# Kernel optimization log

Measured on AMD Instinct MI355X. Metric: run time of the kernel, lower is better.

The kernel has to match this reference:

```python
import jax, jax.numpy as jnp
import numpy as np

# Module hyperparameters (from init_kwargs)
THRESHOLD_BASE = 1.0
TAU_MEM, TAU_SYN, TAU_ADAPT = 0.02, 0.005, 0.1
ADAPT_STRENGTH, HOMEO_RATE, DT = 0.1, 0.01, 0.001


def setup_inputs() -> dict:
    key = jax.random.key(0)
    B, F, T = 32, 8192, 128
    input_current = jax.random.normal(key, (B, F, T), dtype=jnp.float32)
    threshold_scale = jnp.ones((1,), dtype=jnp.float32)   # nn.Parameter(torch.ones(1))
    adaptation_bias = jnp.zeros((1,), dtype=jnp.float32)  # nn.Parameter(torch.zeros(1))
    return {"input_current": input_current,
            "threshold_scale": threshold_scale,
            "adaptation_bias": adaptation_bias}


def reference(input_current, threshold_scale, adaptation_bias):
    """Adaptive-threshold LIF neuron recurrence (AdaptiveThresholdLIFNeuron.forward).

    input_current: [B, F, T]
    Returns (spikes [B,F,T], membrane_trace [T], threshold_trace [T],
             final_firing_rate (scalar EMA), adaptation_state (scalar mean)).
    """
    B, F, T = input_current.shape
    dt = jnp.float32(DT)
    alpha = jnp.exp(-dt / TAU_MEM)   # membrane decay
    beta = jnp.exp(-dt / TAU_SYN)    # synaptic decay
    gamma = jnp.exp(-dt / TAU_ADAPT) # adaptation decay

    I_t = jnp.moveaxis(input_current, -1, 0)  # [T, B, F] for scan over time

    def step(carry, inp):
        membrane, synaptic, adaptation, ema = carry
        synaptic = beta * synaptic + inp
        membrane = alpha * membrane + synaptic
        # homeostatic component uses the running firing-rate EMA (scalar buffer)
        homeo = ADAPT_STRENGTH * jnp.maximum(ema - HOMEO_RATE, 0.0)
        adaptation = gamma * adaptation + (1.0 - gamma) * jax.lax.stop_gradient(membrane)
        threshold = (THRESHOLD_BASE * threshold_scale + homeo
                     + adaptation_bias + 0.1 * adaptation)  # [B, F]
        spike = (membrane >= threshold).astype(membrane.dtype)
        ema = 0.99 * ema + 0.01 * spike.mean()
        membrane = membrane - threshold * spike  # soft reset
        return (membrane, synaptic, adaptation, ema), (spike, membrane.mean(), threshold.mean())

    z = jnp.zeros((B, F), dtype=input_current.dtype)
    init = (z, z, z, jnp.zeros((), dtype=input_current.dtype))
    (membrane, synaptic, adaptation, ema), (spikes_t, mem_trace, thr_trace) = jax.lax.scan(step, init, I_t)

    spikes = jnp.moveaxis(spikes_t, 0, -1)  # [B, F, T]
    return spikes, mem_trace, thr_trace, ema, adaptation.mean()
```

## Files before the change

kernel.cpp:

```cpp
#include <hip/hip_runtime.h>
#include <math.h>

#pragma clang fp contract(off)

typedef unsigned int u32;
typedef unsigned long long u64;

#define N_NEUR 262144
#define TT     128
#define OB     ((size_t)N_NEUR * TT)
#define PB     128
#define PT     512
#define NW     8
#define WGUARD (1 << 16)
#define MGUARD (1 << 17)

__device__ __forceinline__ float wredf(float v) {
#pragma unroll
  for (int o = 32; o; o >>= 1) v += __shfl_xor(v, o);
  return v;
}
__device__ __forceinline__ int wredi(int v) {
#pragma unroll
  for (int o = 32; o; o >>= 1) v += __shfl_xor(v, o);
  return v;
}

__launch_bounds__(PT)
__global__ void snn_persist(const float* __restrict__ in, const float* __restrict__ tsp,
                            const float* __restrict__ abp, float* __restrict__ out,
                            u32* __restrict__ bits2, u32* __restrict__ g_cnt,
                            u64* __restrict__ g_sc, float* __restrict__ wm,
                            float* __restrict__ wt, float* __restrict__ wa)
{
#pragma clang fp contract(off)
  const int tid  = threadIdx.x;
  const int bid  = blockIdx.x;
  const int lane = tid & 63;
  const int wv   = tid >> 6;

  if (bid == PB) {
    if (wv != 0) return;
    const float tsv = tsp[0], abv = abp[0];
    float ema = 0.0f;
    for (int t = 0; t < TT; ++t) {
      const u32* slots = g_cnt + (size_t)t * PB;
      u32 v0, v1; int gd = 0;
      while (1) {
        v0 = __hip_atomic_load(&slots[lane],      __ATOMIC_RELAXED, __HIP_MEMORY_SCOPE_AGENT);
        v1 = __hip_atomic_load(&slots[lane + 64], __ATOMIC_RELAXED, __HIP_MEMORY_SCOPE_AGENT);
        if (__all(v0 != 0u && v1 != 0u)) break;
        if (++gd > MGUARD) break;
      }
      int ss = (int)(v0 ? v0 - 1u : 0u) + (int)(v1 ? v1 - 1u : 0u);
      ss = wredi(ss);
      const float mean = (float)ss * 3.814697265625e-06f;
      ema = __builtin_fmaf(0.99f, ema, 0.01f * mean);
      if (t < TT - 1) {
        const float scn = (tsv + 0.1f * fmaxf(ema - 0.01f, 0.0f)) + abv;
        const u64 pkt = ((u64)__float_as_uint(scn) << 32) | 1ull;
        if (lane < 16)
          __hip_atomic_store(&g_sc[(size_t)(t + 1) * 16 + lane], pkt,
                             __ATOMIC_RELAXED, __HIP_MEMORY_SCOPE_AGENT);
      }
    }
    if (lane == 0) out[OB + 256] = ema;
    return;
  }

  const int gtid = bid * PT + tid;

  const float alp = __uint_as_float(0x3F7383C5u);
  const float bet = __uint_as_float(0x3F519856u);
  const float gma = __uint_as_float(0x3F7D73E8u);
  const float omg = 1.0f - gma;
  const float tsv = tsp[0];
  const float abv = abp[0];

  const int n0 = gtid * 4;
  const float4* q0 = (const float4*)(in + (size_t)(n0 + 0) * TT);
  const float4* q1 = (const float4*)(in + (size_t)(n0 + 1) * TT);
  const float4* q2 = (const float4*)(in + (size_t)(n0 + 2) * TT);
  const float4* q3 = (const float4*)(in + (size_t)(n0 + 3) * TT);

  float4 c0 = q0[0], c1 = q1[0], c2 = q2[0], c3 = q3[0];
  float4 f0 = q0[1], f1 = q1[1], f2 = q2[1], f3 = q3[1];

  float S0,S1,S2,S3, Mp0,Mp1,Mp2,Mp3, A0,A1,A2,A3;
  S0 = __builtin_fmaf(bet, 0.0f, c0.x); Mp0 = __builtin_fmaf(alp, 0.0f, S0);
  A0 = __builtin_fmaf(gma, 0.0f, omg * Mp0);
  S1 = __builtin_fmaf(bet, 0.0f, c1.x); Mp1 = __builtin_fmaf(alp, 0.0f, S1);
  A1 = __builtin_fmaf(gma, 0.0f, omg * Mp1);
  S2 = __builtin_fmaf(bet, 0.0f, c2.x); Mp2 = __builtin_fmaf(alp, 0.0f, S2);
  A2 = __builtin_fmaf(gma, 0.0f, omg * Mp2);
  S3 = __builtin_fmaf(bet, 0.0f, c3.x); Mp3 = __builtin_fmaf(alp, 0.0f, S3);
  A3 = __builtin_fmaf(gma, 0.0f, omg * Mp3);

  float sc;
  { const float homeo = 0.1f * fmaxf(0.0f - 0.01f, 0.0f);
    sc = (tsv + homeo) + abv; }

  __shared__ int   shc[NW];
  __shared__ float shm[NW];
  __shared__ u32   s_sc;

  float M0, M1, M2, M3;

#define STEP(T_, IN0, IN1, IN2, IN3) {                                         \
    if ((T_) > 0) {                                                            \
      if (tid == 0) {                                                          \
        u64 v_; int gd_ = 0;                                                   \
        while (1) {                                                            \
          v_ = __hip_atomic_load(&g_sc[(size_t)(T_) * 16 + (bid & 15)],        \
                                 __ATOMIC_RELAXED, __HIP_MEMORY_SCOPE_AGENT);  \
          if ((u32)v_ != 0u) break;                                            \
          if (++gd_ > WGUARD) break;                                           \
          __builtin_amdgcn_s_sleep(1);                                         \
        }                                                                      \
        s_sc = (u32)(v_ >> 32);                                                \
      }                                                                        \
      __syncthreads();                                                         \
      sc = __uint_as_float(s_sc);                                              \
    }                                                                          \
    const float th0 = __builtin_fmaf(0.1f, A0, sc);                            \
    const float th1 = __builtin_fmaf(0.1f, A1, sc);                            \
    const float th2 = __builtin_fmaf(0.1f, A2, sc);                            \
    const float th3 = __builtin_fmaf(0.1f, A3, sc);                            \
    const bool sp0 = (Mp0 >= th0);  M0 = sp0 ? Mp0 - th0 : Mp0;                \
    const bool sp1 = (Mp1 >= th1);  M1 = sp1 ? Mp1 - th1 : Mp1;                \
    const bool sp2 = (Mp2 >= th2);  M2 = sp2 ? Mp2 - th2 : Mp2;                \
    const bool sp3 = (Mp3 >= th3);  M3 = sp3 ? Mp3 - th3 : Mp3;                \
    int cnt = (int)sp0 + (int)sp1 + (int)sp2 + (int)sp3;                       \
    cnt = wredi(cnt);                                                          \
    if (lane == 0) shc[wv] = cnt;                                              \
    __syncthreads();                                                           \
    if (tid == 0) {                                                            \
      const int bc = ((((((shc[0] + shc[1]) + shc[2]) + shc[3]) + shc[4])      \
                       + shc[5]) + shc[6]) + shc[7];                           \
      __hip_atomic_store(&g_cnt[(size_t)(T_) * PB + bid], (u32)bc + 1u,        \
                         __ATOMIC_RELAXED, __HIP_MEMORY_SCOPE_AGENT);          \
    }                                                                          \
                                       \
    u32 nib = (u32)sp0 | ((u32)sp1 << 1) | ((u32)sp2 << 2) | ((u32)sp3 << 3);  \
    u32 word = nib << (4 * (tid & 7));                                         \
    word |= (u32)__shfl_xor((int)word, 1);                                     \
    word |= (u32)__shfl_xor((int)word, 2);                                     \
    word |= (u32)__shfl_xor((int)word, 4);                                     \
    if ((tid & 7) == 0) bits2[(size_t)(gtid >> 3) * TT + (T_)] = word;         \
    float msum = ((M0 + M1) + M2) + M3;                                        \
    float tsum = ((th0 + th1) + th2) + th3;                                    \
    msum = wredf(msum); tsum = wredf(tsum);                                    \
    if (lane == 0) {                                                           \
      wm[((size_t)(T_) * PB + bid) * NW + wv] = msum;                          \
      wt[((size_t)(T_) * PB + bid) * NW + wv] = tsum;                          \
    }                                                                          \
    if ((T_) < TT - 1) {             \
      S0 = __builtin_fmaf(bet, S0, (IN0));                                     \
      Mp0 = __builtin_fmaf(alp, M0, S0);                                       \
      A0 = __builtin_fmaf(gma, A0, omg * Mp0);                                 \
      S1 = __builtin_fmaf(bet, S1, (IN1));                                     \
      Mp1 = __builtin_fmaf(alp, M1, S1);                                       \
      A1 = __builtin_fmaf(gma, A1, omg * Mp1);                                 \
      S2 = __builtin_fmaf(bet, S2, (IN2));                                     \
      Mp2 = __builtin_fmaf(alp, M2, S2);                                       \
      A2 = __builtin_fmaf(gma, A2, omg * Mp2);                                 \
      S3 = __builtin_fmaf(bet, S3, (IN3));                                     \
      Mp3 = __builtin_fmaf(alp, M3, S3);                                       \
      A3 = __builtin_fmaf(gma, A3, omg * Mp3);                                 \
    }                                                                          \
  }

#pragma unroll 1
  for (int q = 0; q < 32; ++q) {
    float4 p0 = {0,0,0,0}, p1 = {0,0,0,0}, p2 = {0,0,0,0}, p3 = {0,0,0,0};
    if (q < 30) { p0 = q0[q + 2]; p1 = q1[q + 2]; p2 = q2[q + 2]; p3 = q3[q + 2]; }
    const int tb = 4 * q;
    STEP(tb + 0, c0.y, c1.y, c2.y, c3.y)
    STEP(tb + 1, c0.z, c1.z, c2.z, c3.z)
    STEP(tb + 2, c0.w, c1.w, c2.w, c3.w)
    STEP(tb + 3, f0.x, f1.x, f2.x, f3.x)
    c0 = f0; c1 = f1; c2 = f2; c3 = f3;
    f0 = p0; f1 = p1; f2 = p2; f3 = p3;
  }
#undef STEP

  float asum = ((A0 + A1) + A2) + A3;
  asum = wredf(asum);
  if (lane == 0) shm[wv] = asum;
  __syncthreads();
  if (tid == 0) {
    float bs = 0.f;
    for (int w = 0; w < NW; ++w) bs += shm[w];
    wa[bid] = bs;
  }
}

__launch_bounds__(256)
__global__ void snn_finish(const float* __restrict__ wm, const float* __restrict__ wt,
                           const float* __restrict__ wa, float* __restrict__ out)
{
#pragma clang fp contract(off)
  const int tid = threadIdx.x;
  const float inv = 3.814697265625e-06f;
  if (tid < 128) {
    float s = 0.f;
    for (int j = 0; j < PB * NW; ++j) s += wm[(size_t)tid * PB * NW + j];
    out[OB + tid] = s * inv;
  } else {
    const int t = tid - 128;
    float s = 0.f;
    for (int j = 0; j < PB * NW; ++j) s += wt[(size_t)t * PB * NW + j];
    out[OB + 128 + t] = s * inv;
  }
  if (tid == 0) {
    float s = 0.f;
    for (int b = 0; b < PB; ++b) s += wa[b];
    out[OB + 257] = s * inv;
  }
}

__global__ void snn_expand(const u32* __restrict__ bits2, float* __restrict__ outF)
{
  const int gtid = blockIdx.x * blockDim.x + threadIdx.x;
  const int wave = gtid >> 6, lane = gtid & 63;
  const int nwaves = (gridDim.x * blockDim.x) >> 6;
  const int nloc = lane >> 5;
  const int tq   = lane & 31;
  for (int pair = wave; pair < N_NEUR / 2; pair += nwaves) {
    const int n = 2 * pair + nloc;
    const uint4 w = *(const uint4*)(bits2 + (size_t)(n >> 5) * TT + 4 * tq);
    const int b = n & 31;
    float4 f;
    f.x = (float)((w.x >> b) & 1u);
    f.y = (float)((w.y >> b) & 1u);
    f.z = (float)((w.z >> b) & 1u);
    f.w = (float)((w.w >> b) & 1u);
    ((float4*)outF)[(size_t)n * (TT / 4) + tq] = f;
  }
}

extern "C" void kernel_launch(void* const* d_in, const int* in_sizes, int n_in,
                              void* d_out, int out_size, void* d_ws, size_t ws_size,
                              hipStream_t stream)
{
  const float* in  = (const float*)d_in[0];
  const float* tsp = (const float*)d_in[1];
  const float* abp = (const float*)d_in[2];
  float* out = (float*)d_out;
  unsigned char* ws = (unsigned char*)d_ws;

  if (ws_size < 5326000u) return;

  u32*   bits2 = (u32*)(ws);
  float* wm    = (float*)(ws + 4194304);
  float* wt    = (float*)(ws + 4718592);
  u32*   g_cnt = (u32*)(ws + 5242880);
  u64*   g_sc  = (u64*)(ws + 5308416);
  float* wa    = (float*)(ws + 5324800);

  hipMemsetAsync(g_cnt, 0, 81920, stream);

  snn_persist<<<dim3(PB + 1), dim3(PT), 0, stream>>>(in, tsp, abp, out,
                                                     bits2, g_cnt, g_sc, wm, wt, wa);
  snn_finish<<<dim3(1), dim3(256), 0, stream>>>(wm, wt, wa, out);
  snn_expand<<<dim3(2048), dim3(256), 0, stream>>>(bits2, out);
}
```

Measured before the change: 383.2 us.

## Replace master-block EMA broadcast with replicated all-to-all spike count exchange

Drops the dedicated master block that gathered per-block spike counts and broadcast the new threshold scale. Each block now writes its count into 16 replicated slot arrays, and one wavefront per block polls all 128 counts from its replica and computes the EMA locally. This removes one serial hop (gather, then broadcast) from the per-timestep critical path. In exchange it adds more global polling traffic, a larger memset, and an extra __syncthreads per step.

```diff
diff --git a/kernel.cpp b/kernel.cpp
--- a/kernel.cpp
+++ b/kernel.cpp
@@ -4,7 +4,6 @@
 #pragma clang fp contract(off)
 
 typedef unsigned int u32;
-typedef unsigned long long u64;
 
 #define N_NEUR 262144
 #define TT     128
@@ -12,8 +11,8 @@
 #define PB     128
 #define PT     512
 #define NW     8
-#define WGUARD (1 << 16)
-#define MGUARD (1 << 17)
+#define NREP   16
+#define WGUARD (1 << 17)
 
 __device__ __forceinline__ float wredf(float v) {
 #pragma unroll
@@ -29,46 +28,17 @@
 __launch_bounds__(PT)
 __global__ void snn_persist(const float* __restrict__ in, const float* __restrict__ tsp,
                             const float* __restrict__ abp, float* __restrict__ out,
-                            u32* __restrict__ bits2, u32* __restrict__ g_cnt,
-                            u64* __restrict__ g_sc, float* __restrict__ wm,
-                            float* __restrict__ wt, float* __restrict__ wa)
+                            u32* __restrict__ bits2, u32* __restrict__ g_rep,
+                            float* __restrict__ wm, float* __restrict__ wt,
+                            float* __restrict__ wa)
 {
 #pragma clang fp contract(off)
   const int tid  = threadIdx.x;
   const int bid  = blockIdx.x;
+  const int gtid = bid * PT + tid;
   const int lane = tid & 63;
   const int wv   = tid >> 6;
-
-  if (bid == PB) {
-    if (wv != 0) return;
-    const float tsv = tsp[0], abv = abp[0];
-    float ema = 0.0f;
-    for (int t = 0; t < TT; ++t) {
-      const u32* slots = g_cnt + (size_t)t * PB;
-      u32 v0, v1; int gd = 0;
-      while (1) {
-        v0 = __hip_atomic_load(&slots[lane],      __ATOMIC_RELAXED, __HIP_MEMORY_SCOPE_AGENT);
-        v1 = __hip_atomic_load(&slots[lane + 64], __ATOMIC_RELAXED, __HIP_MEMORY_SCOPE_AGENT);
-        if (__all(v0 != 0u && v1 != 0u)) break;
-        if (++gd > MGUARD) break;
-      }
-      int ss = (int)(v0 ? v0 - 1u : 0u) + (int)(v1 ? v1 - 1u : 0u);
-      ss = wredi(ss);
-      const float mean = (float)ss * 3.814697265625e-06f;
-      ema = __builtin_fmaf(0.99f, ema, 0.01f * mean);
-      if (t < TT - 1) {
-        const float scn = (tsv + 0.1f * fmaxf(ema - 0.01f, 0.0f)) + abv;
-        const u64 pkt = ((u64)__float_as_uint(scn) << 32) | 1ull;
-        if (lane < 16)
-          __hip_atomic_store(&g_sc[(size_t)(t + 1) * 16 + lane], pkt,
-                             __ATOMIC_RELAXED, __HIP_MEMORY_SCOPE_AGENT);
-      }
-    }
-    if (lane == 0) out[OB + 256] = ema;
-    return;
-  }
-
-  const int gtid = bid * PT + tid;
+  const int rep  = bid & (NREP - 1);
 
   const float alp = __uint_as_float(0x3F7383C5u);
   const float bet = __uint_as_float(0x3F519856u);
@@ -96,32 +66,16 @@
   S3 = __builtin_fmaf(bet, 0.0f, c3.x); Mp3 = __builtin_fmaf(alp, 0.0f, S3);
   A3 = __builtin_fmaf(gma, 0.0f, omg * Mp3);
 
-  float sc;
-  { const float homeo = 0.1f * fmaxf(0.0f - 0.01f, 0.0f);
-    sc = (tsv + homeo) + abv; }
+  float ema = 0.0f;
+  float sc  = (tsv + 0.1f * fmaxf(0.0f - 0.01f, 0.0f)) + abv;
 
   __shared__ int   shc[NW];
   __shared__ float shm[NW];
-  __shared__ u32   s_sc;
+  __shared__ u32   s_tot;
 
   float M0, M1, M2, M3;
 
 #define STEP(T_, IN0, IN1, IN2, IN3) {                                         \
-    if ((T_) > 0) {                                                            \
-      if (tid == 0) {                                                          \
-        u64 v_; int gd_ = 0;                                                   \
-        while (1) {                                                            \
-          v_ = __hip_atomic_load(&g_sc[(size_t)(T_) * 16 + (bid & 15)],        \
-                                 __ATOMIC_RELAXED, __HIP_MEMORY_SCOPE_AGENT);  \
-          if ((u32)v_ != 0u) break;                                            \
-          if (++gd_ > WGUARD) break;                                           \
-          __builtin_amdgcn_s_sleep(1);                                         \
-        }                                                                      \
-        s_sc = (u32)(v_ >> 32);                                                \
-      }                                                                        \
-      __syncthreads();                                                         \
-      sc = __uint_as_float(s_sc);                                              \
-    }                                                                          \
     const float th0 = __builtin_fmaf(0.1f, A0, sc);                            \
     const float th1 = __builtin_fmaf(0.1f, A1, sc);                            \
     const float th2 = __builtin_fmaf(0.1f, A2, sc);                            \
@@ -134,13 +88,14 @@
     cnt = wredi(cnt);                                                          \
     if (lane == 0) shc[wv] = cnt;                                              \
     __syncthreads();                                                           \
-    if (tid == 0) {                                                            \
+    if (tid < NREP) {   \
       const int bc = ((((((shc[0] + shc[1]) + shc[2]) + shc[3]) + shc[4])      \
                        + shc[5]) + shc[6]) + shc[7];                           \
-      __hip_atomic_store(&g_cnt[(size_t)(T_) * PB + bid], (u32)bc + 1u,        \
+      __hip_atomic_store(&g_rep[((size_t)(T_) * NREP + tid) * PB + bid],       \
+                         (u32)bc + 1u,                                         \
                          __ATOMIC_RELAXED, __HIP_MEMORY_SCOPE_AGENT);          \
     }                                                                          \
-                                       \
+                        \
     u32 nib = (u32)sp0 | ((u32)sp1 << 1) | ((u32)sp2 << 2) | ((u32)sp3 << 3);  \
     u32 word = nib << (4 * (tid & 7));                                         \
     word |= (u32)__shfl_xor((int)word, 1);                                     \
@@ -168,6 +123,26 @@
       Mp3 = __builtin_fmaf(alp, M3, S3);                                       \
       A3 = __builtin_fmaf(gma, A3, omg * Mp3);                                 \
     }                                                                          \
+                        \
+    if (wv == 0) {                                                             \
+      const u32* slots_ = g_rep + ((size_t)(T_) * NREP + rep) * PB;            \
+      u32 v0_, v1_; int gd_ = 0;                                               \
+      while (1) {                                                              \
+        v0_ = __hip_atomic_load(&slots_[lane],      __ATOMIC_RELAXED,          \
+                                __HIP_MEMORY_SCOPE_AGENT);                     \
+        v1_ = __hip_atomic_load(&slots_[lane + 64], __ATOMIC_RELAXED,          \
+                                __HIP_MEMORY_SCOPE_AGENT);                     \
+        if (__all(v0_ != 0u && v1_ != 0u)) break;                              \
+        if (++gd_ > WGUARD) break;                                             \
+      }                                                                        \
+      int ss_ = (int)(v0_ ? v0_ - 1u : 0u) + (int)(v1_ ? v1_ - 1u : 0u);       \
+      ss_ = wredi(ss_);                                                        \
+      if (lane == 0) s_tot = (u32)ss_;                                         \
+    }                                                                          \
+    __syncthreads();                                                           \
+    const float mean_ = (float)s_tot * 3.814697265625e-06f;        \
+    ema = __builtin_fmaf(0.99f, ema, 0.01f * mean_);                           \
+    sc  = (tsv + 0.1f * fmaxf(ema - 0.01f, 0.0f)) + abv;                       \
   }
 
 #pragma unroll 1
@@ -192,6 +167,7 @@
     float bs = 0.f;
     for (int w = 0; w < NW; ++w) bs += shm[w];
     wa[bid] = bs;
+    if (bid == 0) out[OB + 256] = ema;
   }
 }
 
@@ -249,19 +225,18 @@
   float* out = (float*)d_out;
   unsigned char* ws = (unsigned char*)d_ws;
 
-  if (ws_size < 5326000u) return;
+  if (ws_size < 6292000u) return;
 
   u32*   bits2 = (u32*)(ws);
   float* wm    = (float*)(ws + 4194304);
   float* wt    = (float*)(ws + 4718592);
-  u32*   g_cnt = (u32*)(ws + 5242880);
-  u64*   g_sc  = (u64*)(ws + 5308416);
-  float* wa    = (float*)(ws + 5324800);
-
-  hipMemsetAsync(g_cnt, 0, 81920, stream);
-
-  snn_persist<<<dim3(PB + 1), dim3(PT), 0, stream>>>(in, tsp, abp, out,
-                                                     bits2, g_cnt, g_sc, wm, wt, wa);
+  u32*   g_rep = (u32*)(ws + 5242880);
+  float* wa    = (float*)(ws + 6291456);
+
+  hipMemsetAsync(g_rep, 0, 1048576, stream);
+
+  snn_persist<<<dim3(PB), dim3(PT), 0, stream>>>(in, tsp, abp, out,
+                                                 bits2, g_rep, wm, wt, wa);
   snn_finish<<<dim3(1), dim3(256), 0, stream>>>(wm, wt, wa, out);
   snn_expand<<<dim3(2048), dim3(256), 0, stream>>>(bits2, out);
 }
```

Result: faster. 370.4 us (-3.3%).
